# Optimization experiments

Measured on AMD Instinct MI355X. Metric: run time of the kernel, lower is better.

## Reference

```python
import jax, jax.numpy as jnp
import numpy as np

N = 8000       # n_sample (nodes)
F = 128        # n_feature
H = 128        # n_hidden
E = 256000     # edges (avg degree 32)
NPOOL = 3
K = 10         # propagation steps (args.k)
NC = 2         # n_class
ALPHA = 0.0    # Propagation(alpha=0.0)
CENTS = [400, 20, 1]   # node_pool = round(N**(1/NPOOL)) = 20; n_cent = round(prev/20)


def setup_inputs():
    key = jax.random.key(0)
    ks = jax.random.split(key, 40)
    def nrm(i, shape, scale=1.0):
        return jax.random.normal(ks[i], shape, jnp.float32) * scale
    x = nrm(0, (N, F))
    x_cov = nrm(1, (N, F))
    edge_rows = jax.random.randint(ks[2], (E,), 0, N, dtype=jnp.int32)
    edge_cols = jax.random.randint(ks[3], (E,), 0, N, dtype=jnp.int32)
    adj_vals = jax.random.uniform(ks[4], (E,), jnp.float32)
    raw = jax.random.uniform(ks[5], (E,), jnp.float32) + 0.1
    deg = jax.ops.segment_sum(raw, edge_rows, num_segments=N)
    norm_vals = raw / deg[edge_rows]   # row-normalized adjacency values
    inp = dict(x=x, x_cov=x_cov, edge_rows=edge_rows, edge_cols=edge_cols,
               adj_vals=adj_vals, norm_vals=norm_vals,
               bn_gamma=jnp.ones((F,), jnp.float32), bn_beta=jnp.zeros((F,), jnp.float32))
    i = 6
    for p, nc in enumerate(CENTS):
        inp['c%d_W1' % p] = nrm(i, (F, H), F ** -0.5); i += 1
        inp['c%d_b1' % p] = jnp.zeros((H,), jnp.float32)
        inp['c%d_W2' % p] = nrm(i, (H, nc), H ** -0.5); i += 1
        inp['c%d_b2' % p] = jnp.zeros((nc,), jnp.float32)
    inp['mW1'] = nrm(i, (F, H), F ** -0.5); i += 1
    inp['mb1'] = jnp.zeros((H,), jnp.float32)
    inp['a1'] = jnp.full((1,), 0.25, jnp.float32)   # PReLU slope
    inp['mW2'] = nrm(i, (H, H), H ** -0.5); i += 1
    inp['mb2'] = jnp.zeros((H,), jnp.float32)
    inp['a2'] = jnp.full((1,), 0.25, jnp.float32)
    inp['mW3'] = nrm(i, (H, NC), H ** -0.5); i += 1
    inp['mb3'] = jnp.zeros((NC,), jnp.float32)
    return inp


def _node_corr(z):
    # per-node decomposition of torch.corrcoef(z.T).sum(1):
    #   _node_corr(z).sum(0) == corrcoef(z.T).sum(1)
    zc = z - z.mean(0, keepdims=True)
    zc = zc / (jnp.linalg.norm(zc, axis=0, keepdims=True) + 1e-12)
    return zc * zc.sum(1, keepdims=True)   # [n, F]


def reference(x, x_cov, edge_rows, edge_cols, adj_vals, norm_vals, bn_gamma, bn_beta,
              c0_W1, c0_b1, c0_W2, c0_b2, c1_W1, c1_b1, c1_W2, c1_b2,
              c2_W1, c2_b1, c2_W2, c2_b2, mW1, mb1, a1, mW2, mb2, a2, mW3, mb3):
    # BatchNorm1d (training statistics, biased variance, eps=1e-5)
    mu, var = x.mean(0), x.var(0)
    x = (x - mu) / jnp.sqrt(var + 1e-5) * bn_gamma + bn_beta
    x0 = x

    # --- multi-level clustering / pooling (ClusteringLayer) ---
    cl_params = [(c0_W1, c0_b1, c0_W2, c0_b2), (c1_W1, c1_b1, c1_W2, c1_b2),
                 (c2_W1, c2_b1, c2_W2, c2_b2)]
    masks, corrs = [], []
    xc = x_cov
    for W1, b1, W2, b2 in cl_params:
        h = jax.nn.relu(xc @ W1 + b1)
        S = jax.nn.softmax(h @ W2 + b2, axis=-1)        # soft assignment [n_prev, n_cent]
        corrs.append(_node_corr(xc))                     # corr at the input level
        masks.append(S)
        xc = (S.T @ xc) / (S.sum(0)[:, None] + 1e-12)    # pooled centroid features
    corrs.append(_node_corr(x).sum(0))   # == torch.corrcoef(x.T).sum(1), shape [F]

    # --- gains: sigmoid(corr_{i+1} - normalize_adj(mask_i).T @ corr_i) ---
    gains = []
    for i in range(NPOOL):
        rn = masks[i] / (masks[i].sum(1, keepdims=True) + 1e-12)  # row-normalized (symmetric=False)
        gains.append(jax.nn.sigmoid(corrs[i + 1] - rn.T @ corrs[i]))

    # --- per-feature diagonal-masked sparse matmul chains, restricted to adj's edge set ---
    # projector to original nodes: P_i = masks[0] @ ... @ masks[i]
    P = [masks[0]]
    for i in range(1, NPOOL - 1):
        P.append(P[-1] @ masks[i])
    # (M M^T)[r,c] with M = P_i @ diag(g[:,j]) evaluated only on adj edges, all features at once
    def edge_mask(Pi, g):
        return jnp.einsum('ek,ek,kf->ef', Pi[edge_rows], Pi[edge_cols], g * g)  # [E, F]
    ms = [edge_mask(P[i], gains[i]) for i in reversed(range(NPOOL - 1))]  # i = NPOOL-2 .. 0
    ms = jnp.stack(ms, axis=0).transpose(2, 0, 1)   # [F, NPOOL-1, E]

    def per_feature(a, m_steps):   # sequential carry of adj over feature loop (matches torch)
        def inner(ai, mrow):
            ai = ai * mrow          # adj = adj * mask (elementwise on edge values)
            return ai, ai
        a, temps = jax.lax.scan(inner, a, m_steps)
        return a, temps.sum(0)      # adjs[j] = torch.sparse.sum(stack(temp), dim=0)
    _, adjs = jax.lax.scan(per_feature, adj_vals, ms)   # [F, E] edge values

    # --- diffusion propagation: x <- (1-alpha) * norm_adj @ x + alpha * x0, k times ---
    for _ in range(K):
        agg = jax.ops.segment_sum(norm_vals[:, None] * x[edge_cols], edge_rows, num_segments=N)
        x = (1.0 - ALPHA) * agg + ALPHA * x0

    # --- 3-layer MLP with PReLU + log_softmax ---
    prelu = lambda z, a: jnp.where(z >= 0, z, a * z)
    h = prelu(x @ mW1 + mb1, a1)
    h = prelu(h @ mW2 + mb2, a2)
    logits = h @ mW3 + mb3
    return jax.nn.log_softmax(logits, axis=1), adjs
```

## Files before the change

### kernel.cpp

```cpp
#include <hip/hip_runtime.h>
#include <hip/hip_bf16.h>

typedef __hip_bfloat16 bf16;
typedef __attribute__((ext_vector_type(8))) short s16x8;
typedef __attribute__((ext_vector_type(4))) float f32x4;

static constexpr int NN = 8000;
static constexpr int FF = 128;
static constexpr int EE = 256000;
static constexpr int NC0 = 400;
static constexpr int NC1 = 20;

__device__ __forceinline__ float b2f(bf16 v) { return __bfloat162float(v); }
__device__ __forceinline__ bf16 f2b(float v) { return __float2bfloat16(v); }
__device__ __forceinline__ short f2bs(float v) {
    bf16 h = __float2bfloat16(v);
    return __builtin_bit_cast(short, h);
}
__device__ __forceinline__ float ldw(float v) { return v; }
__device__ __forceinline__ float ldw(bf16 v) { return __bfloat162float(v); }

template <int NW>
__device__ __forceinline__ float block_sum(float v, float* sb) {
    #pragma unroll
    for (int o = 32; o > 0; o >>= 1) v += __shfl_down(v, o, 64);
    int t = threadIdx.x;
    if ((t & 63) == 0) sb[t >> 6] = v;
    __syncthreads();
    float s = 0.f;
    #pragma unroll
    for (int i = 0; i < NW; ++i) s += sb[i];
    __syncthreads();
    return s;
}

template <int NW>
__device__ __forceinline__ float block_max(float v, float* sb) {
    #pragma unroll
    for (int o = 32; o > 0; o >>= 1) v = fmaxf(v, __shfl_down(v, o, 64));
    int t = threadIdx.x;
    if ((t & 63) == 0) sb[t >> 6] = v;
    __syncthreads();
    float m = sb[0];
    #pragma unroll
    for (int i = 1; i < NW; ++i) m = fmaxf(m, sb[i]);
    __syncthreads();
    return m;
}

__global__ void k_fill_b16(bf16* __restrict__ p, float v, long n) {
    long i = (long)blockIdx.x * 256 + threadIdx.x;
    long stride = (long)gridDim.x * 256;
    for (; i < n; i += stride) p[i] = f2b(v);
}

__global__ __launch_bounds__(256)
void k_tsplit(const float* __restrict__ src, bf16* __restrict__ dh, bf16* __restrict__ dl,
              bf16* __restrict__ sh, bf16* __restrict__ sl, int M, int N) {
    __shared__ float t[32][33];
    int bx = blockIdx.x * 32, by = blockIdx.y * 32;
    int x = threadIdx.x;
    for (int y = threadIdx.y; y < 32; y += 8) {
        int m = by + y, n = bx + x;
        if (m < M && n < N) {
            float v = src[(long)m * N + n];
            t[y][x] = v;
            if (sh) {
                bf16 h = f2b(v);
                sh[(long)m * N + n] = h;
                sl[(long)m * N + n] = f2b(v - b2f(h));
            }
        }
    }
    __syncthreads();
    for (int y = threadIdx.y; y < 32; y += 8) {
        int n = bx + y, m = by + x;
        if (n < N && m < M) {
            float v = t[x][y];
            bf16 h = f2b(v);
            dh[(long)n * M + m] = h;
            dl[(long)n * M + m] = f2b(v - b2f(h));
        }
    }
}

__global__ __launch_bounds__(256)
void k_cstat(const float* __restrict__ x, const float* __restrict__ xcov,
             float* __restrict__ acc4) {
    __shared__ float sb[4][256];
    int t = threadIdx.x;
    int col = t & 127, half = t >> 7;
    int rend = min(NN, (blockIdx.x + 1) * 80);
    float sx = 0.f, qx = 0.f, sc = 0.f, qc = 0.f;
    for (int r = blockIdx.x * 80 + half; r < rend; r += 2) {
        float v = x[(long)r * FF + col];
        sx += v; qx += v * v;
        float w = xcov[(long)r * FF + col];
        sc += w; qc += w * w;
    }
    sb[0][t] = sx; sb[1][t] = qx; sb[2][t] = sc; sb[3][t] = qc;
    __syncthreads();
    if (t < 128) {
        atomicAdd(&acc4[0 * 128 + col], sb[0][t] + sb[0][t + 128]);
        atomicAdd(&acc4[1 * 128 + col], sb[1][t] + sb[1][t + 128]);
        atomicAdd(&acc4[2 * 128 + col], sb[2][t] + sb[2][t + 128]);
        atomicAdd(&acc4[3 * 128 + col], sb[3][t] + sb[3][t + 128]);
    }
}

__global__ void k_cfin(const float* __restrict__ acc4, const float* __restrict__ gamma,
                       const float* __restrict__ beta, float* __restrict__ bnsc,
                       float* __restrict__ bnsh, float* __restrict__ statmu,
                       float* __restrict__ statin) {
    int f = threadIdx.x;
    float s = acc4[f], q = acc4[128 + f];
    float mu = s / NN;
    float var = q / NN - mu * mu;
    if (var < 0.f) var = 0.f;
    float rstd = 1.f / sqrtf(var + 1e-5f);
    float sc = gamma[f] * rstd;
    bnsc[f] = sc;
    bnsh[f] = beta[f] - mu * sc;
    float s2 = acc4[256 + f], q2 = acc4[384 + f];
    float m2 = s2 / NN;
    float ss = q2 - s2 * m2;
    if (ss < 0.f) ss = 0.f;
    statmu[f] = m2;
    statin[f] = 1.f / (sqrtf(ss) + 1e-12f);
}

__global__ __launch_bounds__(128)
void k_nodecorr(const float* __restrict__ src, const float* __restrict__ mu,
                const float* __restrict__ invn, float* __restrict__ out) {
    __shared__ float sb[2];
    int n = blockIdx.x, t = threadIdx.x;
    float z = (src[n * FF + t] - mu[t]) * invn[t];
    float tot = block_sum<2>(z, sb);
    out[n * FF + t] = z * tot;
}

__global__ __launch_bounds__(256)
void k_softmax(float* __restrict__ p, int N) {
    __shared__ float sb[4];
    float* row = p + (long)blockIdx.x * N;
    int t = threadIdx.x;
    float m = -1e30f;
    for (int i = t; i < N; i += 256) m = fmaxf(m, row[i]);
    m = block_max<4>(m, sb);
    float s = 0.f;
    for (int i = t; i < N; i += 256) { float e = expf(row[i] - m); row[i] = e; s += e; }
    s = block_sum<4>(s, sb);
    float inv = 1.f / s;
    for (int i = t; i < N; i += 256) row[i] *= inv;
}

__global__ __launch_bounds__(256)
void k_softmax_b16(const float* __restrict__ src, bf16* __restrict__ dst, int N) {
    __shared__ float sb[4];
    const float* row = src + (long)blockIdx.x * N;
    bf16* orow = dst + (long)blockIdx.x * N;
    int t = threadIdx.x;
    float v0 = (t < N) ? row[t] : -1e30f;
    float v1 = (256 + t < N) ? row[256 + t] : -1e30f;
    float m = block_max<4>(fmaxf(v0, v1), sb);
    float e0 = (t < N) ? expf(v0 - m) : 0.f;
    float e1 = (256 + t < N) ? expf(v1 - m) : 0.f;
    float s = block_sum<4>(e0 + e1, sb);
    float inv = 1.f / s;
    if (t < N) orow[t] = f2b(e0 * inv);
    if (256 + t < N) orow[256 + t] = f2b(e1 * inv);
}

template <typename T>
__global__ __launch_bounds__(256)
void k_transpose(const T* __restrict__ src, T* __restrict__ dst, float* __restrict__ cs,
                 int M, int N) {
    __shared__ T t[32][33];
    __shared__ float cbuf[8][33];
    int bx = blockIdx.x * 32, by = blockIdx.y * 32;
    int x = threadIdx.x;
    for (int y = threadIdx.y; y < 32; y += 8) {
        int m = by + y, n = bx + x;
        if (m < M && n < N) t[y][x] = src[(long)m * N + n];
    }
    __syncthreads();
    for (int y = threadIdx.y; y < 32; y += 8) {
        int n = bx + y, m = by + x;
        if (n < N && m < M) dst[(long)n * M + m] = t[x][y];
    }
    if (cs) {
        int ty = threadIdx.y;
        int n = bx + x;
        float p = 0.f;
        if (n < N) {
            for (int y = ty; y < 32; y += 8)
                if (by + y < M) p += ldw(t[y][x]);
        }
        cbuf[ty][x] = p;
        __syncthreads();
        if (ty == 0 && n < N) {
            float s = 0.f;
            #pragma unroll
            for (int i = 0; i < 8; ++i) s += cbuf[i][x];
            atomicAdd(&cs[n], s);
        }
    }
}

__global__ __launch_bounds__(256)
void k_gain0a(const float* __restrict__ T0, const float* __restrict__ cs0,
              float* __restrict__ xc1, float* __restrict__ mu, float* __restrict__ invn) {
    __shared__ float sb[4];
    int f = blockIdx.x;
    float s = 0.f, q = 0.f;
    for (int r = threadIdx.x; r < NC0; r += 256) {
        float v = T0[r * 128 + f] / (cs0[r] + 1e-12f);
        xc1[r * 128 + f] = v;
        s += v; q += v * v;
    }
    s = block_sum<4>(s, sb);
    q = block_sum<4>(q, sb);
    if (threadIdx.x == 0) {
        float m = s / NC0;
        float ss = q - s * m;
        if (ss < 0.f) ss = 0.f;
        mu[f] = m;
        invn[f] = 1.f / (sqrtf(ss) + 1e-12f);
    }
}

__global__ __launch_bounds__(128)
void k_gain0b(const float* __restrict__ xc1, const float* __restrict__ mu,
              const float* __restrict__ invn, const float* __restrict__ T1,
              float* __restrict__ corr1, bf16* __restrict__ g0swz) {
    __shared__ float sb[2];
    int k = blockIdx.x, f = threadIdx.x;
    int ch = k >> 5, rem = k & 31, lhi = rem >> 3, ii = rem & 7;
    int idx = (((ch * 8) + (f >> 4)) * 64 + (lhi * 16 + (f & 15))) * 8 + ii;
    if (k >= NC0) { g0swz[idx] = f2b(0.f); return; }
    float z = (xc1[k * 128 + f] - mu[f]) * invn[f];
    float tot = block_sum<2>(z, sb);
    float corr = z * tot;
    corr1[k * 128 + f] = corr;
    float d = corr - T1[k * 128 + f];
    float g = 1.f / (1.f + expf(-d));
    g0swz[idx] = f2b(g * g);
}

__global__ __launch_bounds__(256)
void k_gain1(const float* __restrict__ T2, const float* __restrict__ cs1,
             const float* __restrict__ T3, bf16* __restrict__ g1swz) {
    __shared__ float xs[20][128];
    __shared__ float mu[128], invn[128];
    __shared__ float sb[4];
    int t = threadIdx.x;
    for (int i = t; i < 20 * 128; i += 256) {
        int r = i >> 7;
        xs[r][i & 127] = T2[i] / (cs1[r] + 1e-12f);
    }
    __syncthreads();
    if (t < 128) {
        float s = 0.f, q = 0.f;
        for (int r = 0; r < 20; ++r) { float v = xs[r][t]; s += v; q += v * v; }
        float m = s / 20.f;
        float ss = q - s * m;
        if (ss < 0.f) ss = 0.f;
        mu[t] = m;
        invn[t] = 1.f / (sqrtf(ss) + 1e-12f);
    }
    __syncthreads();
    for (int r = 0; r < 20; ++r) {
        float z = 0.f;
        if (t < 128) z = (xs[r][t] - mu[t]) * invn[t];
        float tot = block_sum<4>(z, sb);
        if (t < 128) {
            float corr = z * tot;
            float d = corr - T3[r * 128 + t];
            float g = 1.f / (1.f + expf(-d));
            int lhi = (r >> 3) & 3, ii = r & 7;
            g1swz[(((t >> 4) * 64) + (lhi * 16 + (t & 15))) * 8 + ii] = f2b(g * g);
        }
    }
    for (int i = t; i < 12 * 128; i += 256) {
        int k = 20 + (i >> 7), f = i & 127;
        int lhi = (k >> 3) & 3, ii = k & 7;
        g1swz[(((f >> 4) * 64) + (lhi * 16 + (f & 15))) * 8 + ii] = f2b(0.f);
    }
}

template <typename AT, typename WT>
__global__ __launch_bounds__(256)
void k_gemm(const AT* __restrict__ A, const WT* __restrict__ W,
            const float* __restrict__ bias, const float* __restrict__ slope,
            float* __restrict__ C, int M, int K, int N, int act) {
    __shared__ float As[16][68];
    __shared__ float Ws[16][68];
    int tid = threadIdx.x;
    int tx = tid & 15, ty = tid >> 4;
    int m0 = blockIdx.x * 64, n0 = blockIdx.y * 64;
    int KS = gridDim.z;
    int kchunk = ((K + KS * 16 - 1) / (KS * 16)) * 16;
    int kbeg = blockIdx.z * kchunk;
    int kend = min(K, kbeg + kchunk);
    float acc[4][4] = {};
    for (int k0 = kbeg; k0 < kend; k0 += 16) {
        __syncthreads();
        for (int idx = tid; idx < 1024; idx += 256) {
            int r = idx >> 4, kk = idx & 15;
            int m = m0 + r, k = k0 + kk;
            As[kk][r] = (m < M && k < kend) ? ldw(A[(long)m * K + k]) : 0.f;
        }
        for (int idx = tid; idx < 1024; idx += 256) {
            int kk = idx >> 6, n = idx & 63;
            int k = k0 + kk, nn = n0 + n;
            float wv = 0.f;
            if (k < kend && nn < N) wv = ldw(W[(long)k * N + nn]);
            Ws[kk][n] = wv;
        }
        __syncthreads();
        #pragma unroll
        for (int kk = 0; kk < 16; ++kk) {
            float4 a4 = *(const float4*)&As[kk][ty * 4];
            float4 b4 = *(const float4*)&Ws[kk][tx * 4];
            float av[4] = {a4.x, a4.y, a4.z, a4.w};
            float bv[4] = {b4.x, b4.y, b4.z, b4.w};
            #pragma unroll
            for (int i = 0; i < 4; ++i)
                #pragma unroll
                for (int j = 0; j < 4; ++j) acc[i][j] += av[i] * bv[j];
        }
    }
    if (KS > 1) {
        #pragma unroll
        for (int i = 0; i < 4; ++i) {
            int m = m0 + ty * 4 + i;
            if (m >= M) continue;
            #pragma unroll
            for (int j = 0; j < 4; ++j) {
                int n = n0 + tx * 4 + j;
                if (n >= N) continue;
                atomicAdd(&C[(long)m * N + n], acc[i][j]);
            }
        }
    } else {
        float sl = slope ? slope[0] : 0.f;
        #pragma unroll
        for (int i = 0; i < 4; ++i) {
            int m = m0 + ty * 4 + i;
            if (m >= M) continue;
            #pragma unroll
            for (int j = 0; j < 4; ++j) {
                int n = n0 + tx * 4 + j;
                if (n >= N) continue;
                float v = acc[i][j] + (bias ? bias[n] : 0.f);
                if (act == 1) v = fmaxf(v, 0.f);
                else if (act == 2) v = (v >= 0.f) ? v : sl * v;
                C[(long)m * N + n] = v;
            }
        }
    }
}

template <int PARTS>
__global__ __launch_bounds__(256)
void k_gmm(const bf16* __restrict__ Ah, const bf16* __restrict__ Al,
           const bf16* __restrict__ BTh, const bf16* __restrict__ BTl,
           const float* __restrict__ bias, const float* __restrict__ slope,
           float* __restrict__ C, bf16* __restrict__ Csh, bf16* __restrict__ Csl,
           int padN, int M, int K, int N, int act) {
    __shared__ __align__(16) short At[2][64 * 40];
    __shared__ __align__(16) short Bt[2][64 * 40];
    int tid = threadIdx.x;
    int m0 = blockIdx.x * 64, n0 = blockIdx.y * 64;
    int KS = gridDim.z;
    int kchunk = ((K + KS * 32 - 1) / (KS * 32)) * 32;
    int kbeg = blockIdx.z * kchunk;
    int kend = min(K, kbeg + kchunk);
    int r = tid >> 2, s = tid & 3;
    int l = tid & 63, w = tid >> 6;
    int c = l & 15, g = l >> 4;
    bool arow_ok = (m0 + r < M);
    bool brow_ok = (n0 + r < N);
    const short* ahp = (const short*)Ah + (long)(m0 + r) * K;
    const short* alp = (PARTS >= 3) ? (const short*)Al + (long)(m0 + r) * K : nullptr;
    const short* bhp = (const short*)BTh + (long)(n0 + r) * K;
    const short* blp = (PARTS >= 2) ? (const short*)BTl + (long)(n0 + r) * K : nullptr;
    short* aw = &At[0][r * 40 + 8 * s];
    short* bw = &Bt[0][r * 40 + 8 * s];
    const int afo = (16 * w + c) * 40 + 8 * g;
    f32x4 acc[4] = {};
    for (int k0 = kbeg; k0 < kend; k0 += 32) {
        __syncthreads();
        {
            int kk = k0 + 8 * s;
            bool kok = kk < kend;
            s16x8 av = {}, bv = {};
            if (arow_ok && kok) av = *(const s16x8*)(ahp + kk);
            if (brow_ok && kok) bv = *(const s16x8*)(bhp + kk);
            *(s16x8*)aw = av;
            *(s16x8*)bw = bv;
            if (PARTS >= 2) {
                s16x8 b2 = {};
                if (brow_ok && kok) b2 = *(const s16x8*)(blp + kk);
                *(s16x8*)(bw + 64 * 40) = b2;
            }
            if (PARTS >= 3) {
                s16x8 a2 = {};
                if (arow_ok && kok) a2 = *(const s16x8*)(alp + kk);
                *(s16x8*)(aw + 64 * 40) = a2;
            }
        }
        __syncthreads();
        s16x8 ah_ = *(const s16x8*)&At[0][afo];
        s16x8 al_;
        if (PARTS >= 3) al_ = *(const s16x8*)&At[1][afo];
        #pragma unroll
        for (int nt = 0; nt < 4; ++nt) {
            int bfo = (16 * nt + c) * 40 + 8 * g;
            s16x8 bh_ = *(const s16x8*)&Bt[0][bfo];
            acc[nt] = __builtin_amdgcn_mfma_f32_16x16x32_bf16(ah_, bh_, acc[nt], 0, 0, 0);
            if (PARTS >= 2) {
                s16x8 bl_ = *(const s16x8*)&Bt[1][bfo];
                acc[nt] = __builtin_amdgcn_mfma_f32_16x16x32_bf16(ah_, bl_, acc[nt], 0, 0, 0);
            }
            if (PARTS >= 3)
                acc[nt] = __builtin_amdgcn_mfma_f32_16x16x32_bf16(al_, bh_, acc[nt], 0, 0, 0);
        }
    }
    if (KS > 1) {
        #pragma unroll
        for (int nt = 0; nt < 4; ++nt) {
            int n = n0 + 16 * nt + c;
            if (n >= N) continue;
            #pragma unroll
            for (int q = 0; q < 4; ++q) {
                int m = m0 + 16 * w + 4 * g + q;
                if (m < M) atomicAdd(&C[(long)m * N + n], acc[nt][q]);
            }
        }
    } else if (Csh && Csl) {
        float sl = slope ? slope[0] : 0.f;
        #pragma unroll
        for (int nt = 0; nt < 4; ++nt) {
            int n = n0 + 16 * nt + c;
            if (n >= N) continue;
            float bv = bias ? bias[n] : 0.f;
            #pragma unroll
            for (int q = 0; q < 4; ++q) {
                int m = m0 + 16 * w + 4 * g + q;
                if (m >= M) continue;
                float v = acc[nt][q] + bv;
                if (act == 1) v = fmaxf(v, 0.f);
                else if (act == 2) v = (v >= 0.f) ? v : sl * v;
                bf16 hi = f2b(v);
                Csh[(long)m * N + n] = hi;
                Csl[(long)m * N + n] = f2b(v - b2f(hi));
            }
        }
    } else if (Csh) {
        #pragma unroll
        for (int nt = 0; nt < 4; ++nt) {
            int n = n0 + 16 * nt + c;
            if (n >= padN) continue;
            float bv = (bias && n < N) ? bias[n] : 0.f;
            #pragma unroll
            for (int q = 0; q < 4; ++q) {
                int m = m0 + 16 * w + 4 * g + q;
                if (m >= M) continue;
                float v = (n < N) ? acc[nt][q] + bv : 0.f;
                Csh[(long)m * padN + n] = f2b(v);
            }
        }
    } else {
        float sl = slope ? slope[0] : 0.f;
        #pragma unroll
        for (int nt = 0; nt < 4; ++nt) {
            int n = n0 + 16 * nt + c;
            if (n >= N) continue;
            float bv = bias ? bias[n] : 0.f;
            #pragma unroll
            for (int q = 0; q < 4; ++q) {
                int m = m0 + 16 * w + 4 * g + q;
                if (m >= M) continue;
                float v = acc[nt][q] + bv;
                if (act == 1) v = fmaxf(v, 0.f);
                else if (act == 2) v = (v >= 0.f) ? v : sl * v;
                C[(long)m * N + n] = v;
            }
        }
    }
}

#define KE_CHUNK(AR, AC, CH)                                                        \
    {                                                                               \
        s16x8 wv;                                                                   \
        _Pragma("unroll")                                                           \
        for (int i = 0; i < 8; ++i) {                                               \
            float av = __uint_as_float(((unsigned)(unsigned short)(AR)[i]) << 16);  \
            float bv = __uint_as_float(((unsigned)(unsigned short)(AC)[i]) << 16);  \
            wv[i] = f2bs(av * bv);                                                  \
        }                                                                           \
        int4 wvi = __builtin_bit_cast(int4, wv);                                    \
        int4 wfi;                                                                   \
        wfi.x = __builtin_amdgcn_ds_bpermute(pa, wvi.x);                            \
        wfi.y = __builtin_amdgcn_ds_bpermute(pa, wvi.y);                            \
        wfi.z = __builtin_amdgcn_ds_bpermute(pa, wvi.z);                            \
        wfi.w = __builtin_amdgcn_ds_bpermute(pa, wvi.w);                            \
        s16x8 wfrag = __builtin_bit_cast(s16x8, wfi);                               \
        const s16x8* gc = g0p + (long)(CH) * 512 + l;                               \
        _Pragma("unroll")                                                           \
        for (int t = 0; t < 8; ++t)                                                 \
            acc0[t] = __builtin_amdgcn_mfma_f32_16x16x32_bf16(gc[t * 64], wfrag, acc0[t], 0, 0, 0); \
    }

__global__ __launch_bounds__(256)
void k_edge(const int* __restrict__ er, const int* __restrict__ ec,
            const float* __restrict__ adj,
            const bf16* __restrict__ S0b, const bf16* __restrict__ P1hp,
            const bf16* __restrict__ g0swz, const bf16* __restrict__ g1swz,
            bf16* __restrict__ outp, int E) {
    __shared__ __align__(16) short Ot[128 * 72];
    const int tid = threadIdx.x;
    const int e0 = blockIdx.x * 64;
    const int l = tid & 63, w = tid >> 6;
    const int c = l & 15, g = l >> 4;
    const int eb = 16 * w + (l >> 2), seg = l & 3;
    const int rn = er[e0 + eb], cn = ec[e0 + eb];
    const short* S0s = (const short*)S0b;
    const short* rrow = S0s + (long)rn * 400 + 8 * seg;
    const short* crow = S0s + (long)cn * 400 + 8 * seg;
    const int pa = ((((l & 15) << 2) + g) << 2);
    const s16x8* g0p = (const s16x8*)g0swz;
    const int ecl = 16 * w + c;
    float pre = adj[e0 + ecl];
    s16x8 pr = {}, pc = {};
    if (seg < 3) {
        const short* P1s = (const short*)P1hp;
        pr = *(const s16x8*)(P1s + (long)rn * 24 + 8 * seg);
        pc = *(const s16x8*)(P1s + (long)cn * 24 + 8 * seg);
    }
    f32x4 acc0[8] = {};
    f32x4 acc1[8] = {};
    s16x8 arA = *(const s16x8*)(rrow);
    s16x8 acA = *(const s16x8*)(crow);
    s16x8 arB = *(const s16x8*)(rrow + 32);
    s16x8 acB = *(const s16x8*)(crow + 32);
    #pragma unroll 1
    for (int ch = 0; ch < 12; ch += 2) {
        s16x8 nar = *(const s16x8*)(rrow + 32 * (ch + 2));
        s16x8 nac = *(const s16x8*)(crow + 32 * (ch + 2));
        KE_CHUNK(arA, acA, ch);
        arA = nar; acA = nac;
        s16x8 nbr = {}, nbc = {};
        if (ch + 3 < 13) {
            nbr = *(const s16x8*)(rrow + 32 * (ch + 3));
            nbc = *(const s16x8*)(crow + 32 * (ch + 3));
        }
        KE_CHUNK(arB, acB, ch + 1);
        arB = nbr; acB = nbc;
    }
    KE_CHUNK(arA, acA, 12);
    {
        s16x8 wv = {};
        if (seg < 3) {
            #pragma unroll
            for (int i = 0; i < 8; ++i) {
                float av = __uint_as_float(((unsigned)(unsigned short)pr[i]) << 16);
                float bv = __uint_as_float(((unsigned)(unsigned short)pc[i]) << 16);
                wv[i] = f2bs(av * bv);
            }
        }
        int4 wvi = __builtin_bit_cast(int4, wv);
        int4 wfi;
        wfi.x = __builtin_amdgcn_ds_bpermute(pa, wvi.x);
        wfi.y = __builtin_amdgcn_ds_bpermute(pa, wvi.y);
        wfi.z = __builtin_amdgcn_ds_bpermute(pa, wvi.z);
        wfi.w = __builtin_amdgcn_ds_bpermute(pa, wvi.w);
        s16x8 wfrag = __builtin_bit_cast(s16x8, wfi);
        const s16x8* g1p = (const s16x8*)g1swz;
        #pragma unroll
        for (int t = 0; t < 8; ++t)
            acc1[t] = __builtin_amdgcn_mfma_f32_16x16x32_bf16(g1p[t * 64 + l], wfrag, acc1[t], 0, 0, 0);
    }
    #pragma unroll
    for (int t = 0; t < 8; ++t) {
        float m10 = acc0[t][0], m11 = acc0[t][1], m12 = acc0[t][2], m13 = acc0[t][3];
        float m00 = acc1[t][0], m01 = acc1[t][1], m02 = acc1[t][2], m03 = acc1[t][3];
        float q0 = m00 * m10, q1 = m01 * m11, q2 = m02 * m12, q3 = m03 * m13;
        float eq1 = q0, eq2 = q0 * q1, eq3 = eq2 * q2;
        float incg = eq3 * q3;
        float u = __shfl_up(incg, 16, 64); if (g >= 1) incg *= u;
        u = __shfl_up(incg, 32, 64); if (g >= 2) incg *= u;
        float exg = __shfl_up(incg, 16, 64); if (g == 0) exg = 1.f;
        float tot = __shfl(incg, 48 + c, 64);
        float base = pre * exg;
        pre *= tot;
        int fb = 16 * t + 4 * g;
        Ot[(fb + 0) * 72 + ecl] = f2bs(base * m00 * (1.f + m10));
        Ot[(fb + 1) * 72 + ecl] = f2bs(base * eq1 * m01 * (1.f + m11));
        Ot[(fb + 2) * 72 + ecl] = f2bs(base * eq2 * m02 * (1.f + m12));
        Ot[(fb + 3) * 72 + ecl] = f2bs(base * eq3 * m03 * (1.f + m13));
    }
    __syncthreads();
    const int fo = tid & 127, hf = tid >> 7;
    if (fo < 127 || e0 < 240000) {
        const short* lsrc = &Ot[fo * 72 + hf * 32];
        short* gdst = (short*)outp + (long)fo * E + e0 + hf * 32;
        #pragma unroll
        for (int q = 0; q < 4; ++q)
            *(s16x8*)(gdst + 8 * q) = *(const s16x8*)(lsrc + 8 * q);
    }
}
#undef KE_CHUNK

__global__ void k_count(const int* __restrict__ er, int* __restrict__ counts, int E) {
    int e = blockIdx.x * 256 + threadIdx.x;
    if (e < E) atomicAdd(&counts[er[e]], 1);
}

__global__ __launch_bounds__(256)
void k_scan(const int* __restrict__ counts, int* __restrict__ rs,
            int* __restrict__ cur, int R) {
    __shared__ int buf[2][256];
    int t = threadIdx.x;
    const int PER = 32;
    int b = t * PER;
    int s = 0;
    for (int i = 0; i < PER; ++i) {
        int idx = b + i;
        if (idx < R) s += counts[idx];
    }
    buf[0][t] = s;
    __syncthreads();
    int src = 0;
    for (int off = 1; off < 256; off <<= 1) {
        int v = buf[src][t];
        if (t >= off) v += buf[src][t - off];
        buf[1 - src][t] = v;
        __syncthreads();
        src = 1 - src;
    }
    int base = (t > 0) ? buf[src][t - 1] : 0;
    for (int i = 0; i < PER; ++i) {
        int idx = b + i;
        if (idx < R) {
            int c = counts[idx];
            rs[idx] = base;
            cur[idx] = base;
            base += c;
        }
    }
    if (t == 255) rs[R] = buf[src][255];
}

__global__ void k_scatter(const int* __restrict__ er, const int* __restrict__ ec,
                          const float* __restrict__ nv, int* __restrict__ cur,
                          int2* __restrict__ cpack, int E) {
    int e = blockIdx.x * 256 + threadIdx.x;
    if (e < E) {
        int r = er[e];
        int p = atomicAdd(&cur[r], 1);
        cpack[p] = make_int2(ec[e], __float_as_int(nv[e]));
    }
}

__global__ __launch_bounds__(256)
void k_spmv4(const int* __restrict__ rs, const int2* __restrict__ cpack,
             const float* __restrict__ xin, float* __restrict__ xout,
             const float* __restrict__ sc4, const float* __restrict__ sh4, int R) {
    int lane = threadIdx.x & 31;
    int r = blockIdx.x * 8 + (threadIdx.x >> 5);
    if (r >= R) return;
    int jb = rs[r], je = rs[r + 1];
    float4 acc = {0.f, 0.f, 0.f, 0.f};
    if (sc4) {
        float4 sc = ((const float4*)sc4)[lane];
        float4 sh = ((const float4*)sh4)[lane];
        int j = jb;
        for (; j + 4 <= je; j += 4) {
            int2 cv0 = cpack[j], cv1 = cpack[j + 1], cv2 = cpack[j + 2], cv3 = cpack[j + 3];
            float4 x0 = ((const float4*)(xin + (long)cv0.x * FF))[lane];
            float4 x1 = ((const float4*)(xin + (long)cv1.x * FF))[lane];
            float4 x2 = ((const float4*)(xin + (long)cv2.x * FF))[lane];
            float4 x3 = ((const float4*)(xin + (long)cv3.x * FF))[lane];
            float v0 = __int_as_float(cv0.y), v1 = __int_as_float(cv1.y);
            float v2 = __int_as_float(cv2.y), v3 = __int_as_float(cv3.y);
            acc.x += v0 * (x0.x * sc.x + sh.x) + v1 * (x1.x * sc.x + sh.x)
                   + v2 * (x2.x * sc.x + sh.x) + v3 * (x3.x * sc.x + sh.x);
            acc.y += v0 * (x0.y * sc.y + sh.y) + v1 * (x1.y * sc.y + sh.y)
                   + v2 * (x2.y * sc.y + sh.y) + v3 * (x3.y * sc.y + sh.y);
            acc.z += v0 * (x0.z * sc.z + sh.z) + v1 * (x1.z * sc.z + sh.z)
                   + v2 * (x2.z * sc.z + sh.z) + v3 * (x3.z * sc.z + sh.z);
            acc.w += v0 * (x0.w * sc.w + sh.w) + v1 * (x1.w * sc.w + sh.w)
                   + v2 * (x2.w * sc.w + sh.w) + v3 * (x3.w * sc.w + sh.w);
        }
        for (; j < je; ++j) {
            int2 cv = cpack[j];
            float v = __int_as_float(cv.y);
            float4 xv = ((const float4*)(xin + (long)cv.x * FF))[lane];
            acc.x += v * (xv.x * sc.x + sh.x);
            acc.y += v * (xv.y * sc.y + sh.y);
            acc.z += v * (xv.z * sc.z + sh.z);
            acc.w += v * (xv.w * sc.w + sh.w);
        }
    } else {
        int j = jb;
        for (; j + 4 <= je; j += 4) {
            int2 cv0 = cpack[j], cv1 = cpack[j + 1], cv2 = cpack[j + 2], cv3 = cpack[j + 3];
            float4 x0 = ((const float4*)(xin + (long)cv0.x * FF))[lane];
            float4 x1 = ((const float4*)(xin + (long)cv1.x * FF))[lane];
            float4 x2 = ((const float4*)(xin + (long)cv2.x * FF))[lane];
            float4 x3 = ((const float4*)(xin + (long)cv3.x * FF))[lane];
            float v0 = __int_as_float(cv0.y), v1 = __int_as_float(cv1.y);
            float v2 = __int_as_float(cv2.y), v3 = __int_as_float(cv3.y);
            acc.x += v0 * x0.x; acc.y += v0 * x0.y; acc.z += v0 * x0.z; acc.w += v0 * x0.w;
            acc.x += v1 * x1.x; acc.y += v1 * x1.y; acc.z += v1 * x1.z; acc.w += v1 * x1.w;
            acc.x += v2 * x2.x; acc.y += v2 * x2.y; acc.z += v2 * x2.z; acc.w += v2 * x2.w;
            acc.x += v3 * x3.x; acc.y += v3 * x3.y; acc.z += v3 * x3.z; acc.w += v3 * x3.w;
        }
        for (; j < je; ++j) {
            int2 cv = cpack[j];
            float v = __int_as_float(cv.y);
            float4 xv = ((const float4*)(xin + (long)cv.x * FF))[lane];
            acc.x += v * xv.x; acc.y += v * xv.y; acc.z += v * xv.z; acc.w += v * xv.w;
        }
    }
    ((float4*)(xout + (long)r * FF))[lane] = acc;
}

__global__ __launch_bounds__(256)
void k_fc128(const float* __restrict__ xin, const float* __restrict__ W,
             const float* __restrict__ b, const float* __restrict__ a,
             float* __restrict__ hout, int nblk) {
    __shared__ float Ws[16384];
    __shared__ float xs[2][128];
    int t = threadIdx.x;
    for (int i = t; i < 16384; i += 256) Ws[i] = W[i];
    float slope = a[0];
    int half = t >> 7, tt = t & 127;
    float bb = b[tt];
    __syncthreads();
    for (int n = blockIdx.x * 2 + half; n < NN; n += nblk * 2) {
        xs[half][tt] = xin[(long)n * FF + tt];
        __syncthreads();
        float a0 = 0.f, a1 = 0.f, a2 = 0.f, a3 = 0.f;
        #pragma unroll 8
        for (int k = 0; k < 128; k += 4) {
            a0 += xs[half][k + 0] * Ws[(k + 0) * 128 + tt];
            a1 += xs[half][k + 1] * Ws[(k + 1) * 128 + tt];
            a2 += xs[half][k + 2] * Ws[(k + 2) * 128 + tt];
            a3 += xs[half][k + 3] * Ws[(k + 3) * 128 + tt];
        }
        float acc = bb + ((a0 + a1) + (a2 + a3));
        hout[(long)n * FF + tt] = (acc >= 0.f) ? acc : slope * acc;
        __syncthreads();
    }
}

__global__ __launch_bounds__(256)
void k_mlp_tail(const float* __restrict__ hin, const float* __restrict__ W2,
                const float* __restrict__ b2, const float* __restrict__ a2,
                const float* __restrict__ W3, const float* __restrict__ b3,
                bf16* __restrict__ outA, bf16* __restrict__ outB, int nblk) {
    __shared__ float Ws[16384];
    __shared__ float xs[2][128];
    __shared__ float red[8];
    int t = threadIdx.x;
    for (int i = t; i < 16384; i += 256) Ws[i] = W2[i];
    float slope = a2[0];
    int half = t >> 7, tt = t & 127;
    float bb = b2[tt];
    float w30 = W3[tt * 2 + 0], w31 = W3[tt * 2 + 1];
    float b30 = b3[0], b31 = b3[1];
    __syncthreads();
    for (int n = blockIdx.x * 2 + half; n < NN; n += nblk * 2) {
        xs[half][tt] = hin[(long)n * FF + tt];
        __syncthreads();
        float a0 = 0.f, a1 = 0.f, a2_ = 0.f, a3 = 0.f;
        #pragma unroll 8
        for (int k = 0; k < 128; k += 4) {
            a0 += xs[half][k + 0] * Ws[(k + 0) * 128 + tt];
            a1 += xs[half][k + 1] * Ws[(k + 1) * 128 + tt];
            a2_ += xs[half][k + 2] * Ws[(k + 2) * 128 + tt];
            a3 += xs[half][k + 3] * Ws[(k + 3) * 128 + tt];
        }
        float acc = bb + ((a0 + a1) + (a2_ + a3));
        float h2 = (acc >= 0.f) ? acc : slope * acc;
        float l0 = h2 * w30, l1 = h2 * w31;
        #pragma unroll
        for (int o = 32; o > 0; o >>= 1) {
            l0 += __shfl_down(l0, o, 64);
            l1 += __shfl_down(l1, o, 64);
        }
        int wid = t >> 6;
        if ((t & 63) == 0) { red[wid] = l0; red[4 + wid] = l1; }
        __syncthreads();
        if (tt == 0) {
            float L0 = red[half * 2] + red[half * 2 + 1] + b30;
            float L1 = red[4 + half * 2] + red[4 + half * 2 + 1] + b31;
            float m = fmaxf(L0, L1);
            float lse = m + logf(expf(L0 - m) + expf(L1 - m));
            bf16 v0 = f2b(L0 - lse), v1 = f2b(L1 - lse);
            outA[n * 2 + 0] = v0; outA[n * 2 + 1] = v1;
            outB[n * 2 + 0] = v0; outB[n * 2 + 1] = v1;
        }
        __syncthreads();
    }
}

extern "C" void kernel_launch(void* const* d_in, const int* in_sizes, int n_in,
                              void* d_out, int out_size, void* d_ws, size_t ws_size,
                              hipStream_t stream) {
    const float* x     = (const float*)d_in[0];
    const float* xcov  = (const float*)d_in[1];
    const int*   erow  = (const int*)d_in[2];
    const int*   ecol  = (const int*)d_in[3];
    const float* adjv  = (const float*)d_in[4];
    const float* normv = (const float*)d_in[5];
    const float* gamma = (const float*)d_in[6];
    const float* beta  = (const float*)d_in[7];
    const float* c0W1 = (const float*)d_in[8];  const float* c0b1 = (const float*)d_in[9];
    const float* c0W2 = (const float*)d_in[10]; const float* c0b2 = (const float*)d_in[11];
    const float* c1W1 = (const float*)d_in[12]; const float* c1b1 = (const float*)d_in[13];
    const float* c1W2 = (const float*)d_in[14]; const float* c1b2 = (const float*)d_in[15];
    const float* mW1 = (const float*)d_in[20]; const float* mb1 = (const float*)d_in[21];
    const float* a1  = (const float*)d_in[22];
    const float* mW2 = (const float*)d_in[23]; const float* mb2 = (const float*)d_in[24];
    const float* a2  = (const float*)d_in[25];
    const float* mW3 = (const float*)d_in[26]; const float* mb3 = (const float*)d_in[27];

    char* B = (char*)d_out;
    bf16* logitsA = (bf16*)B;
    bf16* logitsB = (bf16*)(B + 32000);
    bf16* adjsOut = (bf16*)(B + 64000);

    auto ovl = [](const void* a, size_t an, const void* b, size_t bn) {
        const char* A = (const char*)a; const char* Bp = (const char*)b;
        return (A < Bp + bn) && (Bp < A + an);
    };
    size_t outBytes = (size_t)out_size * 2;
    static const int expSize[28] = {1024000,1024000,256000,256000,256000,256000,128,128,
                                    16384,128,51200,400, 16384,128,2560,20, 16384,128,128,1,
                                    16384,128,1, 16384,128,1, 256,2};
    int code = 0;
    if (n_in != 28) code = 200;
    else for (int i = 0; i < 28 && !code; ++i) if (in_sizes[i] != expSize[i]) code = 200;
    if (!code && ovl(d_ws, ws_size, d_out, outBytes)) code = 300;
    if (!code) {
        for (int i = 0; i < 28; ++i) {
            size_t bytes = (size_t)in_sizes[i] * 4;
            if (ovl(d_ws, ws_size, d_in[i], bytes)) { code = 400; break; }
            if (ovl(d_out, outBytes, d_in[i], bytes)) { code = 500; break; }
        }
    }
    if (!code && ws_size < (size_t)6935040) code = 600;
    if (code) {
        k_fill_b16<<<64, 256, 0, stream>>>(logitsA, (float)code, 16000);
        k_fill_b16<<<64, 256, 0, stream>>>(logitsB, (float)code, 16000);
        k_fill_b16<<<2048, 256, 0, stream>>>(adjsOut, 0.0f, (outBytes - 64000) / 2);
        return;
    }

    char* ws = (char*)d_ws;
    bf16*  S0b   = (bf16*)(ws + 0);
    bf16*  P1hp  = (bf16*)(ws + 6400000);
    bf16*  g0swz = (bf16*)(ws + 6784000);
    bf16*  g1swz = (bf16*)(ws + 6890496);

    char* S = B + 64000;
    float* xbn   = (float*)(S + 0);
    float* ping  = (float*)(S + 4096000);
    float* h0    = (float*)(S + 8192000);
    float* hh2   = (float*)(S + 12288000);
    float* S0f   = (float*)(S + 16384000);
    bf16*  S0Tb  = (bf16*)(S + 29184000);
    int*   rs    = (int*)(S + 36224000);
    int*   cur   = (int*)(S + 36256016);
    int2*  cpack = (int2*)(S + 36288016);
    float* T0    = (float*)(S + 38400512);
    float* T1    = (float*)(S + 38605312);
    float* xc1   = (float*)(S + 38810112);
    float* corr1 = (float*)(S + 39014912);
    float* h1    = (float*)(S + 39219712);
    float* S1    = (float*)(S + 39424512);
    float* S1T   = (float*)(S + 39456512);
    float* T2    = (float*)(S + 39488512);
    float* T3    = (float*)(S + 39498752);
    float* cs0   = (float*)(S + 39529472);
    float* cs1   = (float*)(S + 39531072);
    float* bnsc  = (float*)(S + 39532032);
    float* bnsh  = (float*)(S + 39532544);
    float* statmu= (float*)(S + 39533056);
    float* statin= (float*)(S + 39533568);
    float* acc4  = (float*)(S + 39534080);
    bf16* xcovh  = (bf16*)(S + 39749120);
    bf16* xcovl  = (bf16*)(S + 41797120);
    bf16* xcovTh = (bf16*)(S + 43845120);
    bf16* xcovTl = (bf16*)(S + 45893120);
    bf16* hh2Th  = (bf16*)(S + 47941120);
    bf16* hh2Tl  = (bf16*)(S + 49989120);
    bf16* h0h    = (bf16*)(S + 52037120);
    bf16* h0l    = (bf16*)(S + 54085120);
    bf16* W1Th   = (bf16*)(S + 56133120);
    bf16* W1Tl   = (bf16*)(S + 56165888);
    bf16* W2Th   = (bf16*)(S + 56198656);
    bf16* W2Tl   = (bf16*)(S + 56301056);
    bf16* S1Th   = (bf16*)(S + 56403456);
    bf16* S1Tl   = (bf16*)(S + 56419456);

    hipMemsetAsync(acc4, 0, 4 * 128 * 4, stream);
    k_cstat<<<100, 256, 0, stream>>>(x, xcov, acc4);
    k_cfin<<<1, 128, 0, stream>>>(acc4, gamma, beta, bnsc, bnsh, statmu, statin);
    k_nodecorr<<<NN, 128, 0, stream>>>(xcov, statmu, statin, hh2);
    k_tsplit<<<dim3(4, 250), dim3(32, 8), 0, stream>>>(xcov, xcovTh, xcovTl, xcovh, xcovl, NN, FF);
    k_tsplit<<<dim3(4, 250), dim3(32, 8), 0, stream>>>(hh2, hh2Th, hh2Tl, nullptr, nullptr, NN, FF);
    k_tsplit<<<dim3(4, 4), dim3(32, 8), 0, stream>>>(c0W1, W1Th, W1Tl, nullptr, nullptr, 128, 128);
    k_tsplit<<<dim3(13, 4), dim3(32, 8), 0, stream>>>(c0W2, W2Th, W2Tl, nullptr, nullptr, 128, NC0);
    k_gmm<3><<<dim3(125, 2, 1), 256, 0, stream>>>(xcovh, xcovl, W1Th, W1Tl, c0b1, nullptr,
                                                  nullptr, h0h, h0l, 0, NN, 128, 128, 1);
    k_gmm<3><<<dim3(125, 7, 1), 256, 0, stream>>>(h0h, h0l, W2Th, W2Tl, c0b2, nullptr,
                                                  S0f, nullptr, nullptr, 0, NN, 128, NC0, 0);
    k_softmax_b16<<<NN, 256, 0, stream>>>(S0f, S0b, NC0);
    hipMemsetAsync(cs0, 0, NC0 * 4, stream);
    k_transpose<bf16><<<dim3(13, 250), dim3(32, 8), 0, stream>>>(S0b, S0Tb, cs0, NN, NC0);
    hipMemsetAsync(T0, 0, NC0 * 128 * 4, stream);
    hipMemsetAsync(T1, 0, NC0 * 128 * 4, stream);
    k_gmm<2><<<dim3(7, 2, 16), 256, 0, stream>>>(S0Tb, nullptr, xcovTh, xcovTl, nullptr, nullptr,
                                                 T0, nullptr, nullptr, 0, NC0, NN, 128, 0);
    k_gmm<2><<<dim3(7, 2, 16), 256, 0, stream>>>(S0Tb, nullptr, hh2Th, hh2Tl, nullptr, nullptr,
                                                 T1, nullptr, nullptr, 0, NC0, NN, 128, 0);
    k_gain0a<<<128, 256, 0, stream>>>(T0, cs0, xc1, statmu, statin);
    k_gain0b<<<416, 128, 0, stream>>>(xc1, statmu, statin, T1, corr1, g0swz);
    k_gemm<float, float><<<dim3(7, 2, 1), 256, 0, stream>>>(xc1, c1W1, c1b1, nullptr, h1, NC0, 128, 128, 1);
    k_gemm<float, float><<<dim3(7, 1, 1), 256, 0, stream>>>(h1, c1W2, c1b2, nullptr, S1, NC0, 128, NC1, 0);
    k_softmax<<<NC0, 256, 0, stream>>>(S1, NC1);
    hipMemsetAsync(cs1, 0, NC1 * 4, stream);
    k_transpose<float><<<dim3(1, 13), dim3(32, 8), 0, stream>>>(S1, S1T, cs1, NC0, NC1);
    k_tsplit<<<dim3(1, 13), dim3(32, 8), 0, stream>>>(S1, S1Th, S1Tl, nullptr, nullptr, NC0, NC1);
    hipMemsetAsync(T2, 0, NC1 * 128 * 4, stream);
    hipMemsetAsync(T3, 0, NC1 * 128 * 4, stream);
    k_gemm<float, float><<<dim3(1, 2, 4), 256, 0, stream>>>(S1T, xc1, nullptr, nullptr, T2, NC1, NC0, 128, 0);
    k_gemm<float, float><<<dim3(1, 2, 4), 256, 0, stream>>>(S1T, corr1, nullptr, nullptr, T3, NC1, NC0, 128, 0);
    k_gain1<<<1, 256, 0, stream>>>(T2, cs1, T3, g1swz);
    k_gmm<2><<<dim3(125, 1, 1), 256, 0, stream>>>(S0b, nullptr, S1Th, S1Tl, nullptr, nullptr,
                                                  nullptr, P1hp, nullptr, 24, NN, NC0, NC1, 0);
    hipMemsetAsync(cur, 0, NN * 4, stream);
    k_count<<<1000, 256, 0, stream>>>(erow, cur, EE);
    k_scan<<<1, 256, 0, stream>>>(cur, rs, cur, NN);
    k_scatter<<<1000, 256, 0, stream>>>(erow, ecol, normv, cur, cpack, EE);
    k_spmv4<<<1000, 256, 0, stream>>>(rs, cpack, x, xbn, bnsc, bnsh, NN);
    float* xa = xbn;
    float* xb = ping;
    for (int it = 1; it < 10; ++it) {
        k_spmv4<<<1000, 256, 0, stream>>>(rs, cpack, xa, xb, nullptr, nullptr, NN);
        float* t = xa; xa = xb; xb = t;
    }
    k_fc128<<<250, 256, 0, stream>>>(ping, mW1, mb1, a1, h0, 250);
    k_mlp_tail<<<250, 256, 0, stream>>>(h0, mW2, mb2, a2, mW3, mb3, logitsA, logitsB, 250);
    k_edge<<<EE / 64, 256, 0, stream>>>(erow, ecol, adjv, S0b, P1hp, g0swz, g1swz, adjsOut, EE);
}
```

Baseline: 812.4 us.

## Fuse paired pooling GEMMs sharing the A operand and simplify edge kernel loop

```diff
diff --git a/kernel.cpp b/kernel.cpp
--- a/kernel.cpp
+++ b/kernel.cpp
@@ -356,6 +356,76 @@
                 if (act == 1) v = fmaxf(v, 0.f);
                 else if (act == 2) v = (v >= 0.f) ? v : sl * v;
                 C[(long)m * N + n] = v;
+            }
+        }
+    }
+}
+
+__global__ __launch_bounds__(256)
+void k_gemm2f(const float* __restrict__ A, const float* __restrict__ W1,
+              const float* __restrict__ W2, float* __restrict__ C1,
+              float* __restrict__ C2, int M, int K, int N) {
+    __shared__ float As[16][68];
+    __shared__ float Ws1[16][68];
+    __shared__ float Ws2[16][68];
+    int tid = threadIdx.x;
+    int tx = tid & 15, ty = tid >> 4;
+    int m0 = blockIdx.x * 64, n0 = blockIdx.y * 64;
+    int KS = gridDim.z;
+    int kchunk = ((K + KS * 16 - 1) / (KS * 16)) * 16;
+    int kbeg = blockIdx.z * kchunk;
+    int kend = min(K, kbeg + kchunk);
+    float acc1[4][4] = {}, acc2[4][4] = {};
+    for (int k0 = kbeg; k0 < kend; k0 += 16) {
+        __syncthreads();
+        for (int idx = tid; idx < 1024; idx += 256) {
+            int r = idx >> 4, kk = idx & 15;
+            int m = m0 + r, k = k0 + kk;
+            As[kk][r] = (m < M && k < kend) ? A[(long)m * K + k] : 0.f;
+        }
+        for (int idx = tid; idx < 1024; idx += 256) {
+            int kk = idx >> 6, n = idx & 63;
+            int k = k0 + kk, nn = n0 + n;
+            float w1 = 0.f, w2 = 0.f;
+            if (k < kend && nn < N) {
+                w1 = W1[(long)k * N + nn];
+                w2 = W2[(long)k * N + nn];
+            }
+            Ws1[kk][n] = w1;
+            Ws2[kk][n] = w2;
+        }
+        __syncthreads();
+        #pragma unroll
+        for (int kk = 0; kk < 16; ++kk) {
+            float4 a4 = *(const float4*)&As[kk][ty * 4];
+            float4 b4 = *(const float4*)&Ws1[kk][tx * 4];
+            float4 c4 = *(const float4*)&Ws2[kk][tx * 4];
+            float av[4] = {a4.x, a4.y, a4.z, a4.w};
+            float bv[4] = {b4.x, b4.y, b4.z, b4.w};
+            float cv[4] = {c4.x, c4.y, c4.z, c4.w};
+            #pragma unroll
+            for (int i = 0; i < 4; ++i)
+                #pragma unroll
+                for (int j = 0; j < 4; ++j) {
+                    acc1[i][j] += av[i] * bv[j];
+                    acc2[i][j] += av[i] * cv[j];
+                }
+        }
+    }
+    #pragma unroll
+    for (int i = 0; i < 4; ++i) {
+        int m = m0 + ty * 4 + i;
+        if (m >= M) continue;
+        #pragma unroll
+        for (int j = 0; j < 4; ++j) {
+            int n = n0 + tx * 4 + j;
+            if (n >= N) continue;
+            if (KS > 1) {
+                atomicAdd(&C1[(long)m * N + n], acc1[i][j]);
+                atomicAdd(&C2[(long)m * N + n], acc2[i][j]);
+            } else {
+                C1[(long)m * N + n] = acc1[i][j];
+                C2[(long)m * N + n] = acc2[i][j];
             }
         }
     }
@@ -491,27 +561,85 @@
     }
 }
 
-#define KE_CHUNK(AR, AC, CH)                                                        \
-    {                                                                               \
-        s16x8 wv;                                                                   \
-        _Pragma("unroll")                                                           \
-        for (int i = 0; i < 8; ++i) {                                               \
-            float av = __uint_as_float(((unsigned)(unsigned short)(AR)[i]) << 16);  \
-            float bv = __uint_as_float(((unsigned)(unsigned short)(AC)[i]) << 16);  \
-            wv[i] = f2bs(av * bv);                                                  \
-        }                                                                           \
-        int4 wvi = __builtin_bit_cast(int4, wv);                                    \
-        int4 wfi;                                                                   \
-        wfi.x = __builtin_amdgcn_ds_bpermute(pa, wvi.x);                            \
-        wfi.y = __builtin_amdgcn_ds_bpermute(pa, wvi.y);                            \
-        wfi.z = __builtin_amdgcn_ds_bpermute(pa, wvi.z);                            \
-        wfi.w = __builtin_amdgcn_ds_bpermute(pa, wvi.w);                            \
-        s16x8 wfrag = __builtin_bit_cast(s16x8, wfi);                               \
-        const s16x8* gc = g0p + (long)(CH) * 512 + l;                               \
-        _Pragma("unroll")                                                           \
-        for (int t = 0; t < 8; ++t)                                                 \
-            acc0[t] = __builtin_amdgcn_mfma_f32_16x16x32_bf16(gc[t * 64], wfrag, acc0[t], 0, 0, 0); \
-    }
+__global__ __launch_bounds__(256)
+void k_gmm2(const bf16* __restrict__ Ah,
+            const bf16* __restrict__ B1h, const bf16* __restrict__ B1l,
+            const bf16* __restrict__ B2h, const bf16* __restrict__ B2l,
+            float* __restrict__ C1, float* __restrict__ C2, int M, int K, int N) {
+    __shared__ __align__(16) short At[64 * 40];
+    __shared__ __align__(16) short Bt[4][64 * 40];
+    int tid = threadIdx.x;
+    int m0 = blockIdx.x * 64, n0 = blockIdx.y * 64;
+    int KS = gridDim.z;
+    int kchunk = ((K + KS * 32 - 1) / (KS * 32)) * 32;
+    int kbeg = blockIdx.z * kchunk;
+    int kend = min(K, kbeg + kchunk);
+    int r = tid >> 2, s = tid & 3;
+    int l = tid & 63, w = tid >> 6;
+    int c = l & 15, g = l >> 4;
+    bool arow_ok = (m0 + r < M);
+    bool brow_ok = (n0 + r < N);
+    const short* ahp = (const short*)Ah + (long)(m0 + r) * K;
+    const short* b1hp = (const short*)B1h + (long)(n0 + r) * K;
+    const short* b1lp = (const short*)B1l + (long)(n0 + r) * K;
+    const short* b2hp = (const short*)B2h + (long)(n0 + r) * K;
+    const short* b2lp = (const short*)B2l + (long)(n0 + r) * K;
+    short* aw = &At[r * 40 + 8 * s];
+    short* bw = &Bt[0][r * 40 + 8 * s];
+    const int afo = (16 * w + c) * 40 + 8 * g;
+    f32x4 acc1[4] = {}, acc2[4] = {};
+    for (int k0 = kbeg; k0 < kend; k0 += 32) {
+        __syncthreads();
+        {
+            int kk = k0 + 8 * s;
+            bool kok = kk < kend;
+            s16x8 av = {}, v0 = {}, v1 = {}, v2 = {}, v3 = {};
+            if (arow_ok && kok) av = *(const s16x8*)(ahp + kk);
+            if (brow_ok && kok) {
+                v0 = *(const s16x8*)(b1hp + kk);
+                v1 = *(const s16x8*)(b1lp + kk);
+                v2 = *(const s16x8*)(b2hp + kk);
+                v3 = *(const s16x8*)(b2lp + kk);
+            }
+            *(s16x8*)aw = av;
+            *(s16x8*)(bw + 0 * 2560) = v0;
+            *(s16x8*)(bw + 1 * 2560) = v1;
+            *(s16x8*)(bw + 2 * 2560) = v2;
+            *(s16x8*)(bw + 3 * 2560) = v3;
+        }
+        __syncthreads();
+        s16x8 a_ = *(const s16x8*)&At[afo];
+        #pragma unroll
+        for (int nt = 0; nt < 4; ++nt) {
+            int bfo = (16 * nt + c) * 40 + 8 * g;
+            s16x8 b1h_ = *(const s16x8*)&Bt[0][bfo];
+            s16x8 b1l_ = *(const s16x8*)&Bt[1][bfo];
+            s16x8 b2h_ = *(const s16x8*)&Bt[2][bfo];
+            s16x8 b2l_ = *(const s16x8*)&Bt[3][bfo];
+            acc1[nt] = __builtin_amdgcn_mfma_f32_16x16x32_bf16(a_, b1h_, acc1[nt], 0, 0, 0);
+            acc1[nt] = __builtin_amdgcn_mfma_f32_16x16x32_bf16(a_, b1l_, acc1[nt], 0, 0, 0);
+            acc2[nt] = __builtin_amdgcn_mfma_f32_16x16x32_bf16(a_, b2h_, acc2[nt], 0, 0, 0);
+            acc2[nt] = __builtin_amdgcn_mfma_f32_16x16x32_bf16(a_, b2l_, acc2[nt], 0, 0, 0);
+        }
+    }
+    #pragma unroll
+    for (int nt = 0; nt < 4; ++nt) {
+        int n = n0 + 16 * nt + c;
+        if (n >= N) continue;
+        #pragma unroll
+        for (int q = 0; q < 4; ++q) {
+            int m = m0 + 16 * w + 4 * g + q;
+            if (m >= M) continue;
+            if (KS > 1) {
+                atomicAdd(&C1[(long)m * N + n], acc1[nt][q]);
+                atomicAdd(&C2[(long)m * N + n], acc2[nt][q]);
+            } else {
+                C1[(long)m * N + n] = acc1[nt][q];
+                C2[(long)m * N + n] = acc2[nt][q];
+            }
+        }
+    }
+}
 
 __global__ __launch_bounds__(256)
 void k_edge(const int* __restrict__ er, const int* __restrict__ ec,
@@ -531,38 +659,43 @@
     const short* crow = S0s + (long)cn * 400 + 8 * seg;
     const int pa = ((((l & 15) << 2) + g) << 2);
     const s16x8* g0p = (const s16x8*)g0swz;
-    const int ecl = 16 * w + c;
-    float pre = adj[e0 + ecl];
-    s16x8 pr = {}, pc = {};
-    if (seg < 3) {
-        const short* P1s = (const short*)P1hp;
-        pr = *(const s16x8*)(P1s + (long)rn * 24 + 8 * seg);
-        pc = *(const s16x8*)(P1s + (long)cn * 24 + 8 * seg);
-    }
     f32x4 acc0[8] = {};
     f32x4 acc1[8] = {};
-    s16x8 arA = *(const s16x8*)(rrow);
-    s16x8 acA = *(const s16x8*)(crow);
-    s16x8 arB = *(const s16x8*)(rrow + 32);
-    s16x8 acB = *(const s16x8*)(crow + 32);
+    s16x8 ar = *(const s16x8*)(rrow);
+    s16x8 ac = *(const s16x8*)(crow);
     #pragma unroll 1
-    for (int ch = 0; ch < 12; ch += 2) {
-        s16x8 nar = *(const s16x8*)(rrow + 32 * (ch + 2));
-        s16x8 nac = *(const s16x8*)(crow + 32 * (ch + 2));
-        KE_CHUNK(arA, acA, ch);
-        arA = nar; acA = nac;
-        s16x8 nbr = {}, nbc = {};
-        if (ch + 3 < 13) {
-            nbr = *(const s16x8*)(rrow + 32 * (ch + 3));
-            nbc = *(const s16x8*)(crow + 32 * (ch + 3));
-        }
-        KE_CHUNK(arB, acB, ch + 1);
-        arB = nbr; acB = nbc;
-    }
-    KE_CHUNK(arA, acA, 12);
+    for (int ch = 0; ch < 13; ++ch) {
+        s16x8 nar, nac;
+        if (ch < 12) {
+            nar = *(const s16x8*)(rrow + 32 * (ch + 1));
+            nac = *(const s16x8*)(crow + 32 * (ch + 1));
+        }
+        s16x8 wv;
+        #pragma unroll
+        for (int i = 0; i < 8; ++i) {
+            float av = __uint_as_float(((unsigned)(unsigned short)ar[i]) << 16);
+            float bv = __uint_as_float(((unsigned)(unsigned short)ac[i]) << 16);
+            wv[i] = f2bs(av * bv);
+        }
+        int4 wvi = __builtin_bit_cast(int4, wv);
+        int4 wfi;
+        wfi.x = __builtin_amdgcn_ds_bpermute(pa, wvi.x);
+        wfi.y = __builtin_amdgcn_ds_bpermute(pa, wvi.y);
+        wfi.z = __builtin_amdgcn_ds_bpermute(pa, wvi.z);
+        wfi.w = __builtin_amdgcn_ds_bpermute(pa, wvi.w);
+        s16x8 wfrag = __builtin_bit_cast(s16x8, wfi);
+        const s16x8* gc = g0p + (long)ch * 512 + l;
+        #pragma unroll
+        for (int t = 0; t < 8; ++t)
+            acc0[t] = __builtin_amdgcn_mfma_f32_16x16x32_bf16(gc[t * 64], wfrag, acc0[t], 0, 0, 0);
+        ar = nar; ac = nac;
+    }
     {
         s16x8 wv = {};
         if (seg < 3) {
+            const short* P1s = (const short*)P1hp;
+            s16x8 pr = *(const s16x8*)(P1s + (long)rn * 24 + 8 * seg);
+            s16x8 pc = *(const s16x8*)(P1s + (long)cn * 24 + 8 * seg);
             #pragma unroll
             for (int i = 0; i < 8; ++i) {
                 float av = __uint_as_float(((unsigned)(unsigned short)pr[i]) << 16);
@@ -582,6 +715,8 @@
         for (int t = 0; t < 8; ++t)
             acc1[t] = __builtin_amdgcn_mfma_f32_16x16x32_bf16(g1p[t * 64 + l], wfrag, acc1[t], 0, 0, 0);
     }
+    const int ecl = 16 * w + c;
+    float pre = adj[e0 + ecl];
     #pragma unroll
     for (int t = 0; t < 8; ++t) {
         float m10 = acc0[t][0], m11 = acc0[t][1], m12 = acc0[t][2], m13 = acc0[t][3];
@@ -611,7 +746,6 @@
             *(s16x8*)(gdst + 8 * q) = *(const s16x8*)(lsrc + 8 * q);
     }
 }
-#undef KE_CHUNK
 
 __global__ void k_count(const int* __restrict__ er, int* __restrict__ counts, int E) {
     int e = blockIdx.x * 256 + threadIdx.x;
@@ -925,10 +1059,8 @@
     k_transpose<bf16><<<dim3(13, 250), dim3(32, 8), 0, stream>>>(S0b, S0Tb, cs0, NN, NC0);
     hipMemsetAsync(T0, 0, NC0 * 128 * 4, stream);
     hipMemsetAsync(T1, 0, NC0 * 128 * 4, stream);
-    k_gmm<2><<<dim3(7, 2, 16), 256, 0, stream>>>(S0Tb, nullptr, xcovTh, xcovTl, nullptr, nullptr,
-                                                 T0, nullptr, nullptr, 0, NC0, NN, 128, 0);
-    k_gmm<2><<<dim3(7, 2, 16), 256, 0, stream>>>(S0Tb, nullptr, hh2Th, hh2Tl, nullptr, nullptr,
-                                                 T1, nullptr, nullptr, 0, NC0, NN, 128, 0);
+    k_gmm2<<<dim3(7, 2, 16), 256, 0, stream>>>(S0Tb, xcovTh, xcovTl, hh2Th, hh2Tl,
+                                               T0, T1, NC0, NN, 128);
     k_gain0a<<<128, 256, 0, stream>>>(T0, cs0, xc1, statmu, statin);
     k_gain0b<<<416, 128, 0, stream>>>(xc1, statmu, statin, T1, corr1, g0swz);
     k_gemm<float, float><<<dim3(7, 2, 1), 256, 0, stream>>>(xc1, c1W1, c1b1, nullptr, h1, NC0, 128, 128, 1);
@@ -939,8 +1071,7 @@
     k_tsplit<<<dim3(1, 13), dim3(32, 8), 0, stream>>>(S1, S1Th, S1Tl, nullptr, nullptr, NC0, NC1);
     hipMemsetAsync(T2, 0, NC1 * 128 * 4, stream);
     hipMemsetAsync(T3, 0, NC1 * 128 * 4, stream);
-    k_gemm<float, float><<<dim3(1, 2, 4), 256, 0, stream>>>(S1T, xc1, nullptr, nullptr, T2, NC1, NC0, 128, 0);
-    k_gemm<float, float><<<dim3(1, 2, 4), 256, 0, stream>>>(S1T, corr1, nullptr, nullptr, T3, NC1, NC0, 128, 0);
+    k_gemm2f<<<dim3(1, 2, 4), 256, 0, stream>>>(S1T, xc1, corr1, T2, T3, NC1, NC0, 128);
     k_gain1<<<1, 256, 0, stream>>>(T2, cs1, T3, g1swz);
     k_gmm<2><<<dim3(125, 1, 1), 256, 0, stream>>>(S0b, nullptr, S1Th, S1Tl, nullptr, nullptr,
                                                   nullptr, P1hp, nullptr, 24, NN, NC0, NC1, 0);
```

Result: faster. 766.4 us (-5.7%).
